# Performance work log

Measured on AMD Instinct MI355X. Metric: run time of the kernel, lower is better.

## Reference

```python
import jax, jax.numpy as jnp
import numpy as np

N = 50000      # nodes
E = 800000     # edges (before self loops)
IN = 128       # input feature dim
HID = 64       # hidden channels per head
H = 4          # heads
OUT = 1        # final out channels
D1 = H * HID   # 256, concat feature dim
NEG_SLOPE = 0.2


def _p(k, shape):
    return jax.random.normal(k, shape, jnp.float32) * 0.1


def setup_inputs() -> dict:
    key = jax.random.key(0)
    ks = jax.random.split(key, 32)
    inp = {
        "x": jax.random.normal(ks[0], (N, IN), jnp.float32),
        "edge_index": jax.random.randint(ks[1], (2, E), 0, N, dtype=jnp.int32),
        "batch": jnp.zeros((N,), jnp.int32),
    }
    # layer 0: GATConv(IN -> HID, heads=H, concat) ; Linear(IN -> H*HID)
    inp["cW0"] = _p(ks[2], (IN, H * HID)); inp["cas0"] = _p(ks[3], (H, HID))
    inp["cad0"] = _p(ks[4], (H, HID));     inp["cb0"] = jnp.zeros((D1,), jnp.float32)
    inp["lW0"] = _p(ks[5], (IN, D1));      inp["lb0"] = jnp.zeros((D1,), jnp.float32)
    # layer 1: GATConv(D1 -> HID, heads=H, concat) ; Linear(D1 -> D1)
    inp["cW1"] = _p(ks[6], (D1, H * HID)); inp["cas1"] = _p(ks[7], (H, HID))
    inp["cad1"] = _p(ks[8], (H, HID));     inp["cb1"] = jnp.zeros((D1,), jnp.float32)
    inp["lW1"] = _p(ks[9], (D1, D1));      inp["lb1"] = jnp.zeros((D1,), jnp.float32)
    # layer 2: GATConv(D1 -> OUT, heads=H, concat=False -> mean) ; Linear(D1 -> OUT)
    inp["cW2"] = _p(ks[10], (D1, H * OUT)); inp["cas2"] = _p(ks[11], (H, OUT))
    inp["cad2"] = _p(ks[12], (H, OUT));     inp["cb2"] = jnp.zeros((OUT,), jnp.float32)
    inp["lW2"] = _p(ks[13], (D1, OUT));     inp["lb2"] = jnp.zeros((OUT,), jnp.float32)
    return inp


def gat_conv(x, W, att_src, att_dst, bias, src, dst, out_c, concat):
    """PyG-style GATConv with self loops already included in (src, dst)."""
    n = x.shape[0]
    xl = (x @ W).reshape(n, H, out_c)                  # [N,H,C]
    a_s = (xl * att_src).sum(-1)                       # [N,H]
    a_d = (xl * att_dst).sum(-1)                       # [N,H]
    e = jax.nn.leaky_relu(a_s[src] + a_d[dst], NEG_SLOPE)   # [Et,H]
    # numerically stable segment softmax over destination nodes
    e_max = jax.ops.segment_max(e, dst, num_segments=n)
    ex = jnp.exp(e - e_max[dst])
    denom = jax.ops.segment_sum(ex, dst, num_segments=n)
    alpha = ex / (denom[dst] + 1e-16)                  # [Et,H]
    msg = xl[src] * alpha[..., None]                   # [Et,H,C]
    out = jax.ops.segment_sum(msg, dst, num_segments=n)  # [N,H,C]
    out = out.reshape(n, H * out_c) if concat else out.mean(axis=1)
    return out + bias


def _forward(x, edge_index,
             cW0, cas0, cad0, cb0, lW0, lb0,
             cW1, cas1, cad1, cb1, lW1, lb1,
             cW2, cas2, cad2, cb2, lW2, lb2):
    n = x.shape[0]
    loop = jnp.arange(n, dtype=edge_index.dtype)
    src = jnp.concatenate([edge_index[0], loop])
    dst = jnp.concatenate([edge_index[1], loop])
    h = jax.nn.elu(gat_conv(x, cW0, cas0, cad0, cb0, src, dst, HID, True) + (x @ lW0 + lb0))
    h = jax.nn.elu(gat_conv(h, cW1, cas1, cad1, cb1, src, dst, HID, True) + (h @ lW1 + lb1))
    return gat_conv(h, cW2, cas2, cad2, cb2, src, dst, OUT, False) + (h @ lW2 + lb2)


def reference(x, edge_index, batch,
              cW0, cas0, cad0, cb0, lW0, lb0,
              cW1, cas1, cad1, cb1, lW1, lb1,
              cW2, cas2, cad2, cb2, lW2, lb2):
    return _forward(x, edge_index,
                    cW0, cas0, cad0, cb0, lW0, lb0,
                    cW1, cas1, cad1, cb1, lW1, lb1,
                    cW2, cas2, cad2, cb2, lW2, lb2)
```

## Files before the change

### kernel.cpp

```cpp
#include <hip/hip_runtime.h>
#include <cstddef>
#include <cstdint>

#define NN 50000
#define EE 800000
#define ET_ (EE + NN)

typedef __attribute__((ext_vector_type(8))) short bf16x8;
typedef __attribute__((ext_vector_type(4))) float f32x4;

__device__ __forceinline__ float lrelu_(float x) { return x > 0.f ? x : 0.2f * x; }
__device__ __forceinline__ float elu_(float x)   { return x > 0.f ? x : (__expf(x) - 1.f); }
__device__ __forceinline__ short f2bf(float f) {
    unsigned u = __float_as_uint(f);
    unsigned r = (u + 0x7fffu + ((u >> 16) & 1u)) >> 16;
    return (short)r;
}
__device__ __forceinline__ float bflo(unsigned u) { return __uint_as_float(u << 16); }
__device__ __forceinline__ float bfhi(unsigned u) { return __uint_as_float(u & 0xffff0000u); }

#define GL16(gp, lp) __builtin_amdgcn_global_load_lds( \
    (const __attribute__((address_space(1))) unsigned int*)(gp), \
    (__attribute__((address_space(3))) unsigned int*)(lp), 16, 0, 0)


__global__ __launch_bounds__(256) void degree_k(const int* __restrict__ ei, int* __restrict__ deg) {
    int e = blockIdx.x * blockDim.x + threadIdx.x;
    if (e >= ET_) return;
    int d = (e < EE) ? ei[EE + e] : (e - EE);
    atomicAdd(&deg[d], 1);
}

__global__ __launch_bounds__(1024) void alloc_scan(const int* __restrict__ deg, int* __restrict__ rowptr,
                                                   int* __restrict__ gcnt, int n) {
    __shared__ int s[1024];
    __shared__ int basesh;
    int tid = threadIdx.x;
    int gid = blockIdx.x * 1024 + tid;
    int v = (gid < n) ? deg[gid] : 0;
    s[tid] = v;
    __syncthreads();
    for (int off = 1; off < 1024; off <<= 1) {
        int t = (tid >= off) ? s[tid - off] : 0;
        __syncthreads();
        s[tid] += t;
        __syncthreads();
    }
    if (tid == 1023) basesh = atomicAdd(gcnt, s[1023]);
    __syncthreads();
    if (gid < n) rowptr[gid] = basesh + s[tid] - v;
}

__global__ __launch_bounds__(256) void scatter_k(const int* __restrict__ ei,
                                                 const int* __restrict__ rowptr,
                                                 int* __restrict__ cursor,
                                                 int* __restrict__ csr_src) {
    int e = blockIdx.x * blockDim.x + threadIdx.x;
    if (e >= ET_) return;
    int s, d;
    if (e < EE) { s = ei[e]; d = ei[EE + e]; } else { s = e - EE; d = e - EE; }
    int pos = atomicAdd(&cursor[d], 1);
    csr_src[rowptr[d] + pos] = s;
}


__global__ __launch_bounds__(256) void prep_all(const float* __restrict__ x,
                                                const float* __restrict__ cW0, const float* __restrict__ lW0,
                                                const float* __restrict__ cW1, const float* __restrict__ lW1,
                                                short* __restrict__ xb, short* __restrict__ Wt0,
                                                short* __restrict__ Wt1) {
    int i = blockIdx.x * 256 + threadIdx.x;
    if (i < 1600000) {
        float4 v = *(const float4*)(x + (size_t)i * 4);
        short4 o;
        o.x = f2bf(v.x); o.y = f2bf(v.y); o.z = f2bf(v.z); o.w = f2bf(v.w);
        *(short4*)(xb + (size_t)i * 4) = o;
        return;
    }
    i -= 1600000;
    if (i < 512 * 128) {
        int n = i >> 7, k = i & 127;
        float v = (n < 256) ? cW0[k * 256 + n] : lW0[k * 256 + (n - 256)];
        Wt0[i] = f2bf(v);
        return;
    }
    i -= 512 * 128;
    if (i < 512 * 256) {
        int n = i >> 8, k = i & 255;
        float v = (n < 256) ? cW1[k * 256 + n] : lW1[k * 256 + (n - 256)];
        Wt1[i] = f2bf(v);
    }
}


__global__ __launch_bounds__(256) void gemm_bf16(const short* __restrict__ A,
                                                 const short* __restrict__ Wt,
                                                 const float* __restrict__ biasLin,
                                                 short* __restrict__ XLb,
                                                 short* __restrict__ Hlinb,
                                                 int M, int K) {
    __shared__ short As[2][128 * 32];
    __shared__ short Bs[2][128 * 32];
    const int tid = threadIdx.x;
    const int lane = tid & 63;
    const int wid = tid >> 6;
    const int bm = blockIdx.x * 128;
    const int col0 = blockIdx.y * 128;
    const int wr = wid >> 1, wc = wid & 1;

    f32x4 acc[4][4];
#pragma unroll
    for (int i = 0; i < 4; ++i)
#pragma unroll
        for (int j = 0; j < 4; ++j) acc[i][j] = (f32x4){0.f, 0.f, 0.f, 0.f};

    const int lrow = lane & 15, lk = lane >> 4;

    auto stage = [&](int b, int kk) {
#pragma unroll
        for (int it = 0; it < 2; ++it) {
            const int flat = tid + it * 256;
            const int row = flat >> 2, slot = flat & 3;
            const int ss = slot ^ (row & 3);
            int ar = bm + row; ar = (ar < M) ? ar : (M - 1);
            GL16(A + (size_t)ar * K + kk + ss * 8, &As[b][flat * 8]);
            GL16(Wt + (size_t)(col0 + row) * K + kk + ss * 8, &Bs[b][flat * 8]);
        }
    };

    stage(0, 0);
    int cur = 0;
    for (int k0 = 0; k0 < K; k0 += 32) {
        __syncthreads();
        if (k0 + 32 < K) stage(cur ^ 1, k0 + 32);
        bf16x8 af[4], bfr[4];
#pragma unroll
        for (int mi = 0; mi < 4; ++mi) {
            const int r = wr * 64 + mi * 16 + lrow;
            af[mi] = *(const bf16x8*)(&As[cur][(r * 4 + (lk ^ (r & 3))) * 8]);
        }
#pragma unroll
        for (int ni = 0; ni < 4; ++ni) {
            const int c = wc * 64 + ni * 16 + lrow;
            bfr[ni] = *(const bf16x8*)(&Bs[cur][(c * 4 + (lk ^ (c & 3))) * 8]);
        }
#pragma unroll
        for (int mi = 0; mi < 4; ++mi)
#pragma unroll
            for (int ni = 0; ni < 4; ++ni)
                acc[mi][ni] = __builtin_amdgcn_mfma_f32_16x16x32_bf16(af[mi], bfr[ni], acc[mi][ni], 0, 0, 0);
        cur ^= 1;
    }

    const int lrow4 = (lane >> 4) * 4;
    const bool isLin = (col0 >= 256);
#pragma unroll
    for (int mi = 0; mi < 4; ++mi) {
#pragma unroll
        for (int ni = 0; ni < 4; ++ni) {
            const int col = col0 + wc * 64 + ni * 16 + (lane & 15);
#pragma unroll
            for (int rr = 0; rr < 4; ++rr) {
                const int grow = bm + wr * 64 + mi * 16 + lrow4 + rr;
                if (grow < M) {
                    float v = acc[mi][ni][rr];
                    if (isLin) {
                        const int c = col - 256;
                        Hlinb[(size_t)grow * 256 + c] = f2bf(v + biasLin[c]);
                    } else {
                        XLb[(size_t)grow * 256 + col] = f2bf(v);
                    }
                }
            }
        }
    }
}


__global__ __launch_bounds__(256) void attn_prep(const short* __restrict__ XLb,
                                                 const float* __restrict__ cas,
                                                 const float* __restrict__ cad,
                                                 float* __restrict__ AS,
                                                 float* __restrict__ AD, int n_nodes) {
    int n = (blockIdx.x * blockDim.x + threadIdx.x) >> 6;
    int lane = threadIdx.x & 63;
    if (n >= n_nodes) return;
    uint2 q = *(const uint2*)(XLb + (size_t)n * 256 + lane * 4);
    float x0 = bflo(q.x), x1 = bfhi(q.x);
    float x2 = bflo(q.y), x3 = bfhi(q.y);
    float4 sv = *(const float4*)(cas + lane * 4);
    float4 dv = *(const float4*)(cad + lane * 4);
    float ps = x0 * sv.x + x1 * sv.y + x2 * sv.z + x3 * sv.w;
    float pd = x0 * dv.x + x1 * dv.y + x2 * dv.z + x3 * dv.w;
#pragma unroll
    for (int off = 1; off < 16; off <<= 1) {
        ps += __shfl_xor(ps, off);
        pd += __shfl_xor(pd, off);
    }
    if ((lane & 15) == 0) {
        AS[n * 4 + (lane >> 4)] = ps;
        AD[n * 4 + (lane >> 4)] = pd;
    }
}


__global__ __launch_bounds__(256) void gat_agg(const short* __restrict__ XLb,
                                               const float* __restrict__ AS,
                                               const float* __restrict__ AD,
                                               const int* __restrict__ rowptr,
                                               const int* __restrict__ degarr,
                                               const int* __restrict__ csr_src,
                                               const float* __restrict__ cb,
                                               const short* __restrict__ Hlinb,
                                               short* __restrict__ Hb,
                                               const float* __restrict__ cW2,
                                               const float* __restrict__ lW2,
                                               const float* __restrict__ lb2,
                                               float* __restrict__ XL2,
                                               float* __restrict__ LIN2,
                                               int n_nodes) {
    __shared__ int   sIdx[4][64];
    __shared__ float sExT[4][4][72];

    const int tid = threadIdx.x;
    const int lane = tid & 63;
    const int w = tid >> 6;
    const int n = blockIdx.x * 4 + w;
    if (n >= n_nodes) return;

    const int rs = rowptr[n];
    const int deg = degarr[n];
    const float4 ad4 = *(const float4*)(AD + n * 4);

    const int half = lane >> 5;
    const int l32 = lane & 31;
    const int ch0 = l32 * 8;
    const int h = l32 >> 3;

    float4 acc0 = make_float4(0.f, 0.f, 0.f, 0.f);
    float4 acc1 = make_float4(0.f, 0.f, 0.f, 0.f);
    float d0 = 0.f, d1 = 0.f, d2 = 0.f, d3 = 0.f;

    if (deg <= 64) {
        int sv = 0;
        float c0 = -1e30f, c1 = -1e30f, c2 = -1e30f, c3 = -1e30f;
        if (lane < deg) {
            sv = csr_src[rs + lane];
            float4 a = *(const float4*)(AS + sv * 4);
            c0 = lrelu_(a.x + ad4.x); c1 = lrelu_(a.y + ad4.y);
            c2 = lrelu_(a.z + ad4.z); c3 = lrelu_(a.w + ad4.w);
        }
        float m0 = c0, m1 = c1, m2 = c2, m3 = c3;
#pragma unroll
        for (int off = 32; off > 0; off >>= 1) {
            m0 = fmaxf(m0, __shfl_xor(m0, off));
            m1 = fmaxf(m1, __shfl_xor(m1, off));
            m2 = fmaxf(m2, __shfl_xor(m2, off));
            m3 = fmaxf(m3, __shfl_xor(m3, off));
        }
        float e0 = 0.f, e1 = 0.f, e2 = 0.f, e3 = 0.f;
        if (lane < deg) {
            e0 = __expf(c0 - m0); e1 = __expf(c1 - m1);
            e2 = __expf(c2 - m2); e3 = __expf(c3 - m3);
        }
        sIdx[w][lane] = sv;
        sExT[w][0][lane] = e0; sExT[w][1][lane] = e1;
        sExT[w][2][lane] = e2; sExT[w][3][lane] = e3;
        d0 = e0; d1 = e1; d2 = e2; d3 = e3;
        __builtin_amdgcn_wave_barrier();

        int cpad = (deg + 1) & ~1;
        for (int j = 0; j < cpad; j += 2) {
            int jj = j + half;
            int s = sIdx[w][jj];
            float e = sExT[w][h][jj];
            const uint4 q = *(const uint4*)(XLb + (size_t)s * 256 + ch0);
            acc0.x += e * bflo(q.x); acc0.y += e * bfhi(q.x);
            acc0.z += e * bflo(q.y); acc0.w += e * bfhi(q.y);
            acc1.x += e * bflo(q.z); acc1.y += e * bfhi(q.z);
            acc1.z += e * bflo(q.w); acc1.w += e * bfhi(q.w);
        }
    } else {
        float m0 = -1e30f, m1 = -1e30f, m2 = -1e30f, m3 = -1e30f;
        for (int base = 0; base < deg; base += 64) {
            int idx = base + lane;
            if (idx < deg) {
                int s = csr_src[rs + idx];
                float4 a = *(const float4*)(AS + s * 4);
                m0 = fmaxf(m0, lrelu_(a.x + ad4.x));
                m1 = fmaxf(m1, lrelu_(a.y + ad4.y));
                m2 = fmaxf(m2, lrelu_(a.z + ad4.z));
                m3 = fmaxf(m3, lrelu_(a.w + ad4.w));
            }
        }
#pragma unroll
        for (int off = 32; off > 0; off >>= 1) {
            m0 = fmaxf(m0, __shfl_xor(m0, off));
            m1 = fmaxf(m1, __shfl_xor(m1, off));
            m2 = fmaxf(m2, __shfl_xor(m2, off));
            m3 = fmaxf(m3, __shfl_xor(m3, off));
        }
        for (int base = 0; base < deg; base += 64) {
            int cnt = deg - base; if (cnt > 64) cnt = 64;
            int idx = base + lane;
            int sv = 0;
            float e0 = 0.f, e1 = 0.f, e2 = 0.f, e3 = 0.f;
            if (idx < deg) {
                sv = csr_src[rs + idx];
                float4 a = *(const float4*)(AS + sv * 4);
                e0 = __expf(lrelu_(a.x + ad4.x) - m0);
                e1 = __expf(lrelu_(a.y + ad4.y) - m1);
                e2 = __expf(lrelu_(a.z + ad4.z) - m2);
                e3 = __expf(lrelu_(a.w + ad4.w) - m3);
            }
            sIdx[w][lane] = sv;
            sExT[w][0][lane] = e0; sExT[w][1][lane] = e1;
            sExT[w][2][lane] = e2; sExT[w][3][lane] = e3;
            d0 += e0; d1 += e1; d2 += e2; d3 += e3;
            __builtin_amdgcn_wave_barrier();
            int cpad = (cnt + 1) & ~1;
            for (int j = 0; j < cpad; j += 2) {
                int jj = j + half;
                int s = sIdx[w][jj];
                float e = sExT[w][h][jj];
                const uint4 q = *(const uint4*)(XLb + (size_t)s * 256 + ch0);
                acc0.x += e * bflo(q.x); acc0.y += e * bfhi(q.x);
                acc0.z += e * bflo(q.y); acc0.w += e * bfhi(q.y);
                acc1.x += e * bflo(q.z); acc1.y += e * bfhi(q.z);
                acc1.z += e * bflo(q.w); acc1.w += e * bfhi(q.w);
            }
            __builtin_amdgcn_wave_barrier();
        }
    }

    acc0.x += __shfl_xor(acc0.x, 32); acc0.y += __shfl_xor(acc0.y, 32);
    acc0.z += __shfl_xor(acc0.z, 32); acc0.w += __shfl_xor(acc0.w, 32);
    acc1.x += __shfl_xor(acc1.x, 32); acc1.y += __shfl_xor(acc1.y, 32);
    acc1.z += __shfl_xor(acc1.z, 32); acc1.w += __shfl_xor(acc1.w, 32);
#pragma unroll
    for (int off = 32; off > 0; off >>= 1) {
        d0 += __shfl_xor(d0, off); d1 += __shfl_xor(d1, off);
        d2 += __shfl_xor(d2, off); d3 += __shfl_xor(d3, off);
    }
    float den = (h == 0) ? d0 : (h == 1) ? d1 : (h == 2) ? d2 : d3;
    float inv = 1.f / (den + 1e-16f);

    float v0 = 0.f, v1 = 0.f, v2 = 0.f, v3 = 0.f, v4 = 0.f, v5 = 0.f, v6 = 0.f, v7 = 0.f;
    if (lane < 32) {
        size_t o = (size_t)n * 256 + ch0;
        uint4 hq = *(const uint4*)(Hlinb + o);
        float4 cba = *(const float4*)(cb + ch0);
        float4 cbb = *(const float4*)(cb + ch0 + 4);
        v0 = elu_(acc0.x * inv + cba.x + bflo(hq.x));
        v1 = elu_(acc0.y * inv + cba.y + bfhi(hq.x));
        v2 = elu_(acc0.z * inv + cba.z + bflo(hq.y));
        v3 = elu_(acc0.w * inv + cba.w + bfhi(hq.y));
        v4 = elu_(acc1.x * inv + cbb.x + bflo(hq.z));
        v5 = elu_(acc1.y * inv + cbb.y + bfhi(hq.z));
        v6 = elu_(acc1.z * inv + cbb.z + bflo(hq.w));
        v7 = elu_(acc1.w * inv + cbb.w + bfhi(hq.w));
    }

    if (XL2 != nullptr) {
        float p0 = 0.f, p1 = 0.f, p2 = 0.f, p3 = 0.f, pl = 0.f;
        if (lane < 32) {
            const float vv[8] = {v0, v1, v2, v3, v4, v5, v6, v7};
            float4 lwa = *(const float4*)(lW2 + ch0);
            float4 lwb = *(const float4*)(lW2 + ch0 + 4);
            const float lw[8] = {lwa.x, lwa.y, lwa.z, lwa.w, lwb.x, lwb.y, lwb.z, lwb.w};
#pragma unroll
            for (int j = 0; j < 8; ++j) {
                float4 wv = *(const float4*)(cW2 + (ch0 + j) * 4);
                p0 += vv[j] * wv.x; p1 += vv[j] * wv.y;
                p2 += vv[j] * wv.z; p3 += vv[j] * wv.w;
                pl += vv[j] * lw[j];
            }
        }
#pragma unroll
        for (int off = 16; off > 0; off >>= 1) {
            p0 += __shfl_xor(p0, off); p1 += __shfl_xor(p1, off);
            p2 += __shfl_xor(p2, off); p3 += __shfl_xor(p3, off);
            pl += __shfl_xor(pl, off);
        }
        if (lane == 0) {
            *(float4*)(XL2 + n * 4) = make_float4(p0, p1, p2, p3);
            LIN2[n] = pl + lb2[0];
        }
    } else if (lane < 32) {
        size_t o = (size_t)n * 256 + ch0;
        uint4 ov;
        ov.x = (unsigned)(unsigned short)f2bf(v0) | ((unsigned)(unsigned short)f2bf(v1) << 16);
        ov.y = (unsigned)(unsigned short)f2bf(v2) | ((unsigned)(unsigned short)f2bf(v3) << 16);
        ov.z = (unsigned)(unsigned short)f2bf(v4) | ((unsigned)(unsigned short)f2bf(v5) << 16);
        ov.w = (unsigned)(unsigned short)f2bf(v6) | ((unsigned)(unsigned short)f2bf(v7) << 16);
        *(uint4*)(Hb + o) = ov;
    }
}


__global__ __launch_bounds__(256) void l2_agg(const float* __restrict__ XL2,
                                              const float* __restrict__ LIN2,
                                              const float* __restrict__ cas2,
                                              const float* __restrict__ cad2,
                                              const float* __restrict__ cb2,
                                              const int* __restrict__ rowptr,
                                              const int* __restrict__ degarr,
                                              const int* __restrict__ csr_src,
                                              float* __restrict__ out, int n_nodes) {
    int n = (blockIdx.x * blockDim.x + threadIdx.x) >> 6;
    int lane = threadIdx.x & 63;
    if (n >= n_nodes) return;
    int rs = rowptr[n], re = rs + degarr[n];
    float4 xn = *(const float4*)(XL2 + n * 4);
    float cs0 = cas2[0], cs1 = cas2[1], cs2 = cas2[2], cs3 = cas2[3];
    float cd0 = cad2[0], cd1 = cad2[1], cd2 = cad2[2], cd3 = cad2[3];
    float ad0 = xn.x * cd0, ad1 = xn.y * cd1, ad2 = xn.z * cd2, ad3 = xn.w * cd3;

    float m0 = -1e30f, m1 = -1e30f, m2 = -1e30f, m3 = -1e30f;
    for (int i = rs + lane; i < re; i += 64) {
        int s = csr_src[i];
        float4 xs = *(const float4*)(XL2 + s * 4);
        m0 = fmaxf(m0, lrelu_(xs.x * cs0 + ad0));
        m1 = fmaxf(m1, lrelu_(xs.y * cs1 + ad1));
        m2 = fmaxf(m2, lrelu_(xs.z * cs2 + ad2));
        m3 = fmaxf(m3, lrelu_(xs.w * cs3 + ad3));
    }
#pragma unroll
    for (int off = 32; off > 0; off >>= 1) {
        m0 = fmaxf(m0, __shfl_xor(m0, off));
        m1 = fmaxf(m1, __shfl_xor(m1, off));
        m2 = fmaxf(m2, __shfl_xor(m2, off));
        m3 = fmaxf(m3, __shfl_xor(m3, off));
    }

    float d0 = 0.f, d1 = 0.f, d2 = 0.f, d3 = 0.f;
    float t0 = 0.f, t1 = 0.f, t2 = 0.f, t3 = 0.f;
    for (int i = rs + lane; i < re; i += 64) {
        int s = csr_src[i];
        float4 xs = *(const float4*)(XL2 + s * 4);
        float e0 = __expf(lrelu_(xs.x * cs0 + ad0) - m0);
        float e1 = __expf(lrelu_(xs.y * cs1 + ad1) - m1);
        float e2 = __expf(lrelu_(xs.z * cs2 + ad2) - m2);
        float e3 = __expf(lrelu_(xs.w * cs3 + ad3) - m3);
        d0 += e0; d1 += e1; d2 += e2; d3 += e3;
        t0 += e0 * xs.x; t1 += e1 * xs.y; t2 += e2 * xs.z; t3 += e3 * xs.w;
    }
#pragma unroll
    for (int off = 32; off > 0; off >>= 1) {
        d0 += __shfl_xor(d0, off); d1 += __shfl_xor(d1, off);
        d2 += __shfl_xor(d2, off); d3 += __shfl_xor(d3, off);
        t0 += __shfl_xor(t0, off); t1 += __shfl_xor(t1, off);
        t2 += __shfl_xor(t2, off); t3 += __shfl_xor(t3, off);
    }
    if (lane == 0) {
        float r = 0.25f * (t0 / (d0 + 1e-16f) + t1 / (d1 + 1e-16f) +
                           t2 / (d2 + 1e-16f) + t3 / (d3 + 1e-16f));
        out[n] = r + cb2[0] + LIN2[n];
    }
}


extern "C" void kernel_launch(void* const* d_in, const int* in_sizes, int n_in,
                              void* d_out, int out_size, void* d_ws, size_t ws_size,
                              hipStream_t stream) {
    const float* x    = (const float*)d_in[0];
    const int*   ei   = (const int*)d_in[1];
    const float* cW0  = (const float*)d_in[3];
    const float* cas0 = (const float*)d_in[4];
    const float* cad0 = (const float*)d_in[5];
    const float* cb0  = (const float*)d_in[6];
    const float* lW0  = (const float*)d_in[7];
    const float* lb0  = (const float*)d_in[8];
    const float* cW1  = (const float*)d_in[9];
    const float* cas1 = (const float*)d_in[10];
    const float* cad1 = (const float*)d_in[11];
    const float* cb1  = (const float*)d_in[12];
    const float* lW1  = (const float*)d_in[13];
    const float* lb1  = (const float*)d_in[14];
    const float* cW2  = (const float*)d_in[15];
    const float* cas2 = (const float*)d_in[16];
    const float* cad2 = (const float*)d_in[17];
    const float* cb2  = (const float*)d_in[18];
    const float* lW2  = (const float*)d_in[19];
    const float* lb2  = (const float*)d_in[20];
    float* out = (float*)d_out;

    short* xb    = (short*)d_ws;
    short* XLb   = xb + 6400000;
    short* HAb   = XLb + 12800000;
    short* Hlinb = HAb + 12800000;
    short* Wt0   = Hlinb + 12800000;
    short* Wt1   = Wt0 + 65536;
    float* AS    = (float*)(Wt1 + 131072);
    float* AD    = AS + 200000;
    float* XL2   = AD + 200000;
    float* LIN2  = XL2 + 200000;
    int* deg     = (int*)(LIN2 + NN);
    int* cursor  = deg + NN;
    int* gcnt    = cursor + NN;
    int* rowptr  = gcnt + 4;
    int* csr_src = rowptr + NN;

    dim3 b256(256);
    dim3 gEdges((ET_ + 255) / 256);
    dim3 gNodesWave((NN + 3) / 4);

    hipMemsetAsync(deg, 0, (2 * (size_t)NN + 4) * sizeof(int), stream);
    prep_all<<<dim3(7018), b256, 0, stream>>>(x, cW0, lW0, cW1, lW1, xb, Wt0, Wt1);
    degree_k<<<gEdges, b256, 0, stream>>>(ei, deg);
    alloc_scan<<<dim3((NN + 1023) / 1024), dim3(1024), 0, stream>>>(deg, rowptr, gcnt, NN);
    scatter_k<<<gEdges, b256, 0, stream>>>(ei, rowptr, cursor, csr_src);

    dim3 gemmGrid((NN + 127) / 128, 4);

    gemm_bf16<<<gemmGrid, b256, 0, stream>>>(xb, Wt0, lb0, XLb, Hlinb, NN, 128);
    attn_prep<<<gNodesWave, b256, 0, stream>>>(XLb, cas0, cad0, AS, AD, NN);
    gat_agg<<<gNodesWave, b256, 0, stream>>>(XLb, AS, AD, rowptr, deg, csr_src, cb0, Hlinb,
                                             HAb, nullptr, nullptr, nullptr, nullptr, nullptr, NN);

    gemm_bf16<<<gemmGrid, b256, 0, stream>>>(HAb, Wt1, lb1, XLb, Hlinb, NN, 256);
    attn_prep<<<gNodesWave, b256, 0, stream>>>(XLb, cas1, cad1, AS, AD, NN);
    gat_agg<<<gNodesWave, b256, 0, stream>>>(XLb, AS, AD, rowptr, deg, csr_src, cb1, Hlinb,
                                             nullptr, cW2, lW2, lb2, XL2, LIN2, NN);

    l2_agg<<<gNodesWave, b256, 0, stream>>>(XL2, LIN2, cas2, cad2, cb2, rowptr, deg, csr_src, out, NN);
}
```

Measured before the change: 507.0 us.

## Fuse degree count into prep, stage GEMM epilogue via LDS, unroll gather loop

Three separate changes. The degree-count kernel is folded into the prep kernel to save one launch. The GEMM epilogue now writes bf16 results into a swizzled LDS tile and then stores 16-byte row segments to global memory, replacing scattered 2-byte stores and hoisting the bias loads out of the loop. The low-degree aggregation loop is unrolled by four so that several gathers are in flight at once. These add an extra barrier and LDS round trip in the GEMM, and some register pressure in the aggregation kernel.

```diff
diff --git a/kernel.cpp b/kernel.cpp
--- a/kernel.cpp
+++ b/kernel.cpp
@@ -24,12 +24,41 @@
     (__attribute__((address_space(3))) unsigned int*)(lp), 16, 0, 0)
 
 
-__global__ __launch_bounds__(256) void degree_k(const int* __restrict__ ei, int* __restrict__ deg) {
-    int e = blockIdx.x * blockDim.x + threadIdx.x;
-    if (e >= ET_) return;
-    int d = (e < EE) ? ei[EE + e] : (e - EE);
-    atomicAdd(&deg[d], 1);
-}
+__global__ __launch_bounds__(256) void prep_all(const float* __restrict__ x,
+                                                const float* __restrict__ cW0, const float* __restrict__ lW0,
+                                                const float* __restrict__ cW1, const float* __restrict__ lW1,
+                                                const int* __restrict__ ei, int* __restrict__ deg,
+                                                short* __restrict__ xb, short* __restrict__ Wt0,
+                                                short* __restrict__ Wt1) {
+    int i = blockIdx.x * 256 + threadIdx.x;
+    if (i < 1600000) {
+        float4 v = *(const float4*)(x + (size_t)i * 4);
+        short4 o;
+        o.x = f2bf(v.x); o.y = f2bf(v.y); o.z = f2bf(v.z); o.w = f2bf(v.w);
+        *(short4*)(xb + (size_t)i * 4) = o;
+        return;
+    }
+    i -= 1600000;
+    if (i < 512 * 128) {
+        int n = i >> 7, k = i & 127;
+        float v = (n < 256) ? cW0[k * 256 + n] : lW0[k * 256 + (n - 256)];
+        Wt0[i] = f2bf(v);
+        return;
+    }
+    i -= 512 * 128;
+    if (i < 512 * 256) {
+        int n = i >> 8, k = i & 255;
+        float v = (n < 256) ? cW1[k * 256 + n] : lW1[k * 256 + (n - 256)];
+        Wt1[i] = f2bf(v);
+        return;
+    }
+    i -= 512 * 256;
+    if (i < ET_) {
+        int d = (i < EE) ? ei[EE + i] : (i - EE);
+        atomicAdd(&deg[d], 1);
+    }
+}
+
 
 __global__ __launch_bounds__(1024) void alloc_scan(const int* __restrict__ deg, int* __restrict__ rowptr,
                                                    int* __restrict__ gcnt, int n) {
@@ -64,43 +93,13 @@
 }
 
 
-__global__ __launch_bounds__(256) void prep_all(const float* __restrict__ x,
-                                                const float* __restrict__ cW0, const float* __restrict__ lW0,
-                                                const float* __restrict__ cW1, const float* __restrict__ lW1,
-                                                short* __restrict__ xb, short* __restrict__ Wt0,
-                                                short* __restrict__ Wt1) {
-    int i = blockIdx.x * 256 + threadIdx.x;
-    if (i < 1600000) {
-        float4 v = *(const float4*)(x + (size_t)i * 4);
-        short4 o;
-        o.x = f2bf(v.x); o.y = f2bf(v.y); o.z = f2bf(v.z); o.w = f2bf(v.w);
-        *(short4*)(xb + (size_t)i * 4) = o;
-        return;
-    }
-    i -= 1600000;
-    if (i < 512 * 128) {
-        int n = i >> 7, k = i & 127;
-        float v = (n < 256) ? cW0[k * 256 + n] : lW0[k * 256 + (n - 256)];
-        Wt0[i] = f2bf(v);
-        return;
-    }
-    i -= 512 * 128;
-    if (i < 512 * 256) {
-        int n = i >> 8, k = i & 255;
-        float v = (n < 256) ? cW1[k * 256 + n] : lW1[k * 256 + (n - 256)];
-        Wt1[i] = f2bf(v);
-    }
-}
-
-
 __global__ __launch_bounds__(256) void gemm_bf16(const short* __restrict__ A,
                                                  const short* __restrict__ Wt,
                                                  const float* __restrict__ biasLin,
                                                  short* __restrict__ XLb,
                                                  short* __restrict__ Hlinb,
                                                  int M, int K) {
-    __shared__ short As[2][128 * 32];
-    __shared__ short Bs[2][128 * 32];
+    __shared__ short smem[4][128 * 32];
     const int tid = threadIdx.x;
     const int lane = tid & 63;
     const int wid = tid >> 6;
@@ -123,8 +122,8 @@
             const int row = flat >> 2, slot = flat & 3;
             const int ss = slot ^ (row & 3);
             int ar = bm + row; ar = (ar < M) ? ar : (M - 1);
-            GL16(A + (size_t)ar * K + kk + ss * 8, &As[b][flat * 8]);
-            GL16(Wt + (size_t)(col0 + row) * K + kk + ss * 8, &Bs[b][flat * 8]);
+            GL16(A + (size_t)ar * K + kk + ss * 8, &smem[b][flat * 8]);
+            GL16(Wt + (size_t)(col0 + row) * K + kk + ss * 8, &smem[2 + b][flat * 8]);
         }
     };
 
@@ -137,12 +136,12 @@
 #pragma unroll
         for (int mi = 0; mi < 4; ++mi) {
             const int r = wr * 64 + mi * 16 + lrow;
-            af[mi] = *(const bf16x8*)(&As[cur][(r * 4 + (lk ^ (r & 3))) * 8]);
+            af[mi] = *(const bf16x8*)(&smem[cur][(r * 4 + (lk ^ (r & 3))) * 8]);
         }
 #pragma unroll
         for (int ni = 0; ni < 4; ++ni) {
             const int c = wc * 64 + ni * 16 + lrow;
-            bfr[ni] = *(const bf16x8*)(&Bs[cur][(c * 4 + (lk ^ (c & 3))) * 8]);
+            bfr[ni] = *(const bf16x8*)(&smem[2 + cur][(c * 4 + (lk ^ (c & 3))) * 8]);
         }
 #pragma unroll
         for (int mi = 0; mi < 4; ++mi)
@@ -152,26 +151,41 @@
         cur ^= 1;
     }
 
-    const int lrow4 = (lane >> 4) * 4;
+    __syncthreads();
+    short* Ct = &smem[0][0];
     const bool isLin = (col0 >= 256);
+    float bni[4] = {0.f, 0.f, 0.f, 0.f};
+    if (isLin) {
+#pragma unroll
+        for (int ni = 0; ni < 4; ++ni)
+            bni[ni] = biasLin[col0 - 256 + wc * 64 + ni * 16 + lrow];
+    }
+    const int lrow4 = lk * 4;
 #pragma unroll
     for (int mi = 0; mi < 4; ++mi) {
 #pragma unroll
         for (int ni = 0; ni < 4; ++ni) {
-            const int col = col0 + wc * 64 + ni * 16 + (lane & 15);
+            const int col_l = wc * 64 + ni * 16 + lrow;
 #pragma unroll
             for (int rr = 0; rr < 4; ++rr) {
-                const int grow = bm + wr * 64 + mi * 16 + lrow4 + rr;
-                if (grow < M) {
-                    float v = acc[mi][ni][rr];
-                    if (isLin) {
-                        const int c = col - 256;
-                        Hlinb[(size_t)grow * 256 + c] = f2bf(v + biasLin[c]);
-                    } else {
-                        XLb[(size_t)grow * 256 + col] = f2bf(v);
-                    }
-                }
+                const int row_l = wr * 64 + mi * 16 + lrow4 + rr;
+                const int idx = (row_l * 128 + col_l) ^ (((row_l >> 2) & 3) << 4);
+                Ct[idx] = f2bf(acc[mi][ni][rr] + bni[ni]);
             }
+        }
+    }
+    __syncthreads();
+
+    short* outp = isLin ? Hlinb : XLb;
+    const int gcol0 = isLin ? (col0 - 256) : col0;
+#pragma unroll
+    for (int rr8 = 0; rr8 < 8; ++rr8) {
+        const int flat = tid + rr8 * 256;
+        const int row = flat >> 4, seg = flat & 15;
+        const int sidx = (row * 128 + seg * 8) ^ (((row >> 2) & 3) << 4);
+        if (bm + row < M) {
+            bf16x8 vv = *(const bf16x8*)(Ct + sidx);
+            *(bf16x8*)(outp + (size_t)(bm + row) * 256 + gcol0 + seg * 8) = vv;
         }
     }
 }
@@ -241,6 +255,13 @@
     float4 acc1 = make_float4(0.f, 0.f, 0.f, 0.f);
     float d0 = 0.f, d1 = 0.f, d2 = 0.f, d3 = 0.f;
 
+    auto ACC = [&](const uint4& q, float e) {
+        acc0.x += e * bflo(q.x); acc0.y += e * bfhi(q.x);
+        acc0.z += e * bflo(q.y); acc0.w += e * bfhi(q.y);
+        acc1.x += e * bflo(q.z); acc1.y += e * bfhi(q.z);
+        acc1.z += e * bflo(q.w); acc1.w += e * bfhi(q.w);
+    };
+
     if (deg <= 64) {
         int sv = 0;
         float c0 = -1e30f, c1 = -1e30f, c2 = -1e30f, c3 = -1e30f;
@@ -269,16 +290,25 @@
         d0 = e0; d1 = e1; d2 = e2; d3 = e3;
         __builtin_amdgcn_wave_barrier();
 
-        int cpad = (deg + 1) & ~1;
-        for (int j = 0; j < cpad; j += 2) {
+        const int cpad = (deg + 1) & ~1;
+        int j = 0;
+        for (; j + 8 <= cpad; j += 8) {
+            int ja = j + half, jb = j + 2 + half, jc = j + 4 + half, jd = j + 6 + half;
+            int sa = sIdx[w][ja], sb = sIdx[w][jb], sc = sIdx[w][jc], sd = sIdx[w][jd];
+            float ea = sExT[w][h][ja], eb = sExT[w][h][jb];
+            float ec = sExT[w][h][jc], ed = sExT[w][h][jd];
+            uint4 qa = *(const uint4*)(XLb + (size_t)sa * 256 + ch0);
+            uint4 qb = *(const uint4*)(XLb + (size_t)sb * 256 + ch0);
+            uint4 qc = *(const uint4*)(XLb + (size_t)sc * 256 + ch0);
+            uint4 qd = *(const uint4*)(XLb + (size_t)sd * 256 + ch0);
+            ACC(qa, ea); ACC(qb, eb); ACC(qc, ec); ACC(qd, ed);
+        }
+        for (; j < cpad; j += 2) {
             int jj = j + half;
             int s = sIdx[w][jj];
             float e = sExT[w][h][jj];
-            const uint4 q = *(const uint4*)(XLb + (size_t)s * 256 + ch0);
-            acc0.x += e * bflo(q.x); acc0.y += e * bfhi(q.x);
-            acc0.z += e * bflo(q.y); acc0.w += e * bfhi(q.y);
-            acc1.x += e * bflo(q.z); acc1.y += e * bfhi(q.z);
-            acc1.z += e * bflo(q.w); acc1.w += e * bfhi(q.w);
+            uint4 q = *(const uint4*)(XLb + (size_t)s * 256 + ch0);
+            ACC(q, e);
         }
     } else {
         float m0 = -1e30f, m1 = -1e30f, m2 = -1e30f, m3 = -1e30f;
@@ -323,11 +353,8 @@
                 int jj = j + half;
                 int s = sIdx[w][jj];
                 float e = sExT[w][h][jj];
-                const uint4 q = *(const uint4*)(XLb + (size_t)s * 256 + ch0);
-                acc0.x += e * bflo(q.x); acc0.y += e * bfhi(q.x);
-                acc0.z += e * bflo(q.y); acc0.w += e * bfhi(q.y);
-                acc1.x += e * bflo(q.z); acc1.y += e * bfhi(q.z);
-                acc1.z += e * bflo(q.w); acc1.w += e * bfhi(q.w);
+                uint4 q = *(const uint4*)(XLb + (size_t)s * 256 + ch0);
+                ACC(q, e);
             }
             __builtin_amdgcn_wave_barrier();
         }
@@ -506,8 +533,7 @@
     dim3 gNodesWave((NN + 3) / 4);
 
     hipMemsetAsync(deg, 0, (2 * (size_t)NN + 4) * sizeof(int), stream);
-    prep_all<<<dim3(7018), b256, 0, stream>>>(x, cW0, lW0, cW1, lW1, xb, Wt0, Wt1);
-    degree_k<<<gEdges, b256, 0, stream>>>(ei, deg);
+    prep_all<<<dim3(10339), b256, 0, stream>>>(x, cW0, lW0, cW1, lW1, ei, deg, xb, Wt0, Wt1);
     alloc_scan<<<dim3((NN + 1023) / 1024), dim3(1024), 0, stream>>>(deg, rowptr, gcnt, NN);
     scatter_k<<<gEdges, b256, 0, stream>>>(ei, rowptr, cursor, csr_src);
 
```

Result: faster. 462.2 us (-8.8%).
